# Kernel optimization log

Hardware: AMD Instinct MI355X
Metric: run time of the kernel (lower is better)

The kernel has to match this reference:

```python
import jax, jax.numpy as jnp
import numpy as np

B, S, D, H = 2, 2048, 1024, 16
DK = D // H


def setup_inputs() -> dict:
    key = jax.random.key(0)
    ks = jax.random.split(key, 12)
    sd = 1.0 / np.sqrt(D)
    inp = {
        "query": jax.random.normal(ks[0], (B, S, D), jnp.float32),
        "key": jax.random.normal(ks[1], (B, S, D), jnp.float32),
        "value": jax.random.normal(ks[2], (B, S, D), jnp.float32),
        # causal mask, broadcast over batch and heads: [1, 1, S, S]
        "mask": jnp.tril(jnp.ones((S, S), jnp.bool_))[None, None],
        "wq_w": jax.random.uniform(ks[3], (D, D), jnp.float32, -sd, sd),
        "wq_b": jax.random.uniform(ks[4], (D,), jnp.float32, -sd, sd),
        "wk_w": jax.random.uniform(ks[5], (D, D), jnp.float32, -sd, sd),
        "wk_b": jax.random.uniform(ks[6], (D,), jnp.float32, -sd, sd),
        "wv_w": jax.random.uniform(ks[7], (D, D), jnp.float32, -sd, sd),
        "wv_b": jax.random.uniform(ks[8], (D,), jnp.float32, -sd, sd),
        "wo_w": jax.random.uniform(ks[9], (D, D), jnp.float32, -sd, sd),
        "wo_b": jax.random.uniform(ks[10], (D,), jnp.float32, -sd, sd),
    }
    return inp


def reference(query, key, value, mask, wq_w, wq_b, wk_w, wk_b, wv_w, wv_b, wo_w, wo_b):
    # linear projections (torch Linear: x @ W^T + b), split into heads -> [B, H, S, DK]
    def proj(x, w, b):
        y = jnp.einsum("bsd,ed->bse", x, w) + b
        return y.reshape(B, S, H, DK).transpose(0, 2, 1, 3)

    q = proj(query, wq_w, wq_b)
    k = proj(key, wk_w, wk_b)
    v = proj(value, wv_w, wv_b)

    scale = 1.0 / np.sqrt(DK)
    scores = jnp.einsum("bhqd,bhkd->bhqk", q, k) * scale  # [B, H, S, S]
    scores = jnp.where(mask, scores, -jnp.inf)
    attn = jax.nn.softmax(scores, axis=-1)
    out = jnp.einsum("bhqk,bhkd->bhqd", attn, v)  # [B, H, S, DK]
    out = out.transpose(0, 2, 1, 3).reshape(B, S, D)
    # output projection; dropout is identity at eval / p=0
    return jnp.einsum("bsd,ed->bse", out, wo_w) + wo_b
```

## Files before the change

### kernel.cpp

```cpp
#include <hip/hip_runtime.h>


typedef unsigned short u16;
typedef unsigned int u32;
typedef __bf16 bf16x8 __attribute__((ext_vector_type(8)));
typedef float f32x4 __attribute__((ext_vector_type(4)));
typedef float f32x16 __attribute__((ext_vector_type(16)));
typedef float f32x4v __attribute__((ext_vector_type(4)));
typedef u16 u16x4 __attribute__((ext_vector_type(4)));
typedef u32 u32x4 __attribute__((ext_vector_type(4)));
typedef int i32x4 __attribute__((ext_vector_type(4)));

#define B_ 2
#define S_ 2048
#define D_ 1024
#define H_ 16
#define DK_ 64

__device__ __forceinline__ u16 f2bf(float f) {
  __bf16 h = (__bf16)f;
  return __builtin_bit_cast(u16, h);
}
__device__ __forceinline__ float fexp2(float x) { return __builtin_amdgcn_exp2f(x); }

__device__ __forceinline__ f32x4 mfma16(bf16x8 a, bf16x8 b, f32x4 c) {
  return __builtin_amdgcn_mfma_f32_16x16x32_bf16(a, b, c, 0, 0, 0);
}
__device__ __forceinline__ f32x16 mfma32(bf16x8 a, bf16x8 b, f32x16 c) {
  return __builtin_amdgcn_mfma_f32_32x32x16_bf16(a, b, c, 0, 0, 0);
}
__device__ __forceinline__ u32 cvtpk(float lo, float hi) {
  u32 r;
  asm volatile("v_cvt_pk_bf16_f32 %0, %1, %2" : "=v"(r) : "v"(lo), "v"(hi));
  return r;
}
__device__ __forceinline__ u32 sx32(u32 v) { return (u32)__shfl_xor((int)v, 32, 64); }

typedef __attribute__((address_space(1))) void GV;
typedef __attribute__((address_space(3))) void LV;
__device__ __forceinline__ void gload16(const u16* g, u16* l) {
  __builtin_amdgcn_global_load_lds((GV*)g, (LV*)l, 16, 0, 0);
}

__global__ __launch_bounds__(256) void cast_all(const float* __restrict__ s0, const float* __restrict__ s1,
                                                const float* __restrict__ s2, const float* __restrict__ s3,
                                                const float* __restrict__ s4, const float* __restrict__ s5,
                                                const float* __restrict__ s6, u16* __restrict__ dst) {
  const int N0 = 1048576, N1 = 2097152, N2 = 3145728, N3 = 3407872, N4 = 3670016, N5 = 3932160, N6 = 4194304;
  int stride = gridDim.x * blockDim.x;
  for (int i = blockIdx.x * blockDim.x + threadIdx.x; i < N6; i += stride) {
    const float* src;
    int off;
    if (i < N0)      { src = s0; off = i; }
    else if (i < N1) { src = s1; off = i - N0; }
    else if (i < N2) { src = s2; off = i - N1; }
    else if (i < N3) { src = s3; off = i - N2; }
    else if (i < N4) { src = s4; off = i - N3; }
    else if (i < N5) { src = s5; off = i - N4; }
    else             { src = s6; off = i - N5; }
    f32x4v v = reinterpret_cast<const f32x4v*>(src)[off];
    u16x4 o;
    o.x = f2bf(v.x); o.y = f2bf(v.y); o.z = f2bf(v.z); o.w = f2bf(v.w);
    reinterpret_cast<u16x4*>(dst)[i] = o;
  }
}

__device__ __forceinline__ void gemm_tile_128(const u16* __restrict__ A,
                                              const u16* __restrict__ Bw,
                                              int K, int bm, int bn,
                                              f32x4 (&acc)[4][4],
                                              u16* ldsA, u16* ldsB) {
  const int tid = threadIdx.x;
  const int lane = tid & 63;
  const int w = tid >> 6;
  const int wm = w >> 1, wn = w & 1;
  const int fr = lane & 15, fq = lane >> 4;

  const u16* aBase = A + (size_t)(bm * 128) * K;
  const u16* bBase = Bw + (size_t)(bn * 128) * K;

  const int r0 = tid >> 2;
  const int cq0 = tid & 3;
  const int cs0 = (cq0 ^ (r0 & 3)) * 8;
  const int cs1 = (cq0 ^ ((r0 + 64) & 3)) * 8;

#define STAGE_G(buf, kk)                                                                          \
  do {                                                                                            \
    gload16(aBase + (size_t)r0 * K + (kk) + cs0, ldsA + (buf) * 4096 + tid * 8);                  \
    gload16(aBase + (size_t)(r0 + 64) * K + (kk) + cs1, ldsA + (buf) * 4096 + (tid + 256) * 8);   \
    gload16(bBase + (size_t)r0 * K + (kk) + cs0, ldsB + (buf) * 4096 + tid * 8);                  \
    gload16(bBase + (size_t)(r0 + 64) * K + (kk) + cs1, ldsB + (buf) * 4096 + (tid + 256) * 8);   \
  } while (0)

  STAGE_G(0, 0);
  STAGE_G(1, 32);

  const int nk = K >> 5;
  for (int t = 0; t < nk; ++t) {
    if (t + 1 < nk) { asm volatile("s_waitcnt vmcnt(4)" ::: "memory"); }
    else            { asm volatile("s_waitcnt vmcnt(0)" ::: "memory"); }
    __builtin_amdgcn_s_barrier();
    __builtin_amdgcn_sched_barrier(0);
    if (t + 2 < nk) {
      const int nb = (t + 2) % 3;
      STAGE_G(nb, (t + 2) * 32);
    }
    const u16* la = ldsA + (t % 3) * 4096;
    const u16* lb = ldsB + (t % 3) * 4096;
    bf16x8 af[4], bfv[4];
#pragma unroll
    for (int m = 0; m < 4; ++m) {
      int row = wm * 64 + m * 16 + fr;
      int cq = fq ^ (row & 3);
      af[m] = *reinterpret_cast<const bf16x8*>(la + (row * 4 + cq) * 8);
    }
#pragma unroll
    for (int n = 0; n < 4; ++n) {
      int row = wn * 64 + n * 16 + fr;
      int cq = fq ^ (row & 3);
      bfv[n] = *reinterpret_cast<const bf16x8*>(lb + (row * 4 + cq) * 8);
    }
    __builtin_amdgcn_s_setprio(1);
#pragma unroll
    for (int m = 0; m < 4; ++m)
#pragma unroll
      for (int n = 0; n < 4; ++n)
        acc[m][n] = mfma16(af[m], bfv[n], acc[m][n]);
    __builtin_amdgcn_s_setprio(0);
  }
#undef STAGE_G
}

__global__ __launch_bounds__(256) void gemm_qkv(const u16* __restrict__ Xq, const u16* __restrict__ Xk,
                                                const u16* __restrict__ Xv, const u16* __restrict__ Wq,
                                                const u16* __restrict__ Wk, const u16* __restrict__ Wv,
                                                const float* __restrict__ bq, const float* __restrict__ bk,
                                                const float* __restrict__ bv,
                                                u16* __restrict__ Qw, u16* __restrict__ Kw,
                                                u16* __restrict__ Vt) {
  __shared__ __align__(16) u16 lds[6 * 128 * 32];
  u16* ldsA = lds;
  u16* ldsB = lds + 3 * 128 * 32;

  const int id = blockIdx.x;
  const int xcd = id & 7;
  const int l = id >> 3;
  const int bx = l & 7;
  const int g = xcd * 12 + (l >> 3);
  const int z = g >> 5;
  const int by = g & 31;

  const u16* A = (z == 0) ? Xq : (z == 1) ? Xk : Xv;
  const u16* W = (z == 0) ? Wq : (z == 1) ? Wk : Wv;
  const float* bias = (z == 0) ? bq : (z == 1) ? bk : bv;
  const float osc = (z == 0) ? (0.125f * 1.44269504f) : 1.0f;

  f32x4 acc[4][4];
#pragma unroll
  for (int m = 0; m < 4; ++m)
#pragma unroll
    for (int n = 0; n < 4; ++n)
      acc[m][n] = (f32x4){0.f, 0.f, 0.f, 0.f};

  gemm_tile_128(A, W, 1024, by, bx, acc, ldsA, ldsB);

  const int tid = threadIdx.x;
  const int lane = tid & 63;
  const int w = tid >> 6, wm = w >> 1, wn = w & 1;
  const int fr = lane & 15, fq = lane >> 4;

  __syncthreads();

  if (z < 2) {
#pragma unroll
    for (int m = 0; m < 4; ++m)
#pragma unroll
      for (int n = 0; n < 4; ++n) {
        int col = wn * 64 + n * 16 + fr;
        float bcol = bias[bx * 128 + col];
#pragma unroll
        for (int j = 0; j < 4; ++j) {
          int row = wm * 64 + m * 16 + fq * 4 + j;
          lds[row * 128 + col] = f2bf((acc[m][n][j] + bcol) * osc);
        }
      }
    __syncthreads();
    u16* dst = (z == 0) ? Qw : Kw;
#pragma unroll
    for (int p = 0; p < 8; ++p) {
      int lrow = p * 16 + (tid >> 4);
      int lseg = tid & 15;
      i32x4 v = *reinterpret_cast<const i32x4*>(&lds[lrow * 128 + lseg * 8]);
      int grow = by * 128 + lrow;
      int b = grow >> 11, s = grow & (S_ - 1);
      int h = bx * 2 + (lseg >> 3);
      int dk = (lseg & 7) * 8;
      *reinterpret_cast<i32x4*>(&dst[((size_t)(b * H_ + h) * S_ + s) * DK_ + dk]) = v;
    }
  } else {
#pragma unroll
    for (int m = 0; m < 4; ++m)
#pragma unroll
      for (int n = 0; n < 4; ++n) {
        int col = wn * 64 + n * 16 + fr;
        float bcol = bias[bx * 128 + col];
        int row0 = wm * 64 + m * 16 + fq * 4;
        u16x4 pk;
#pragma unroll
        for (int j = 0; j < 4; ++j) pk[j] = f2bf(acc[m][n][j] + bcol);
        *reinterpret_cast<u16x4*>(&lds[col * 136 + row0]) = pk;
      }
    __syncthreads();
#pragma unroll
    for (int p = 0; p < 8; ++p) {
      int dkl = p * 16 + (tid >> 4);
      int seg = tid & 15;
      i32x4 v = *reinterpret_cast<const i32x4*>(&lds[dkl * 136 + seg * 8]);
      int grow = by * 128 + seg * 8;
      int b = grow >> 11, s = grow & (S_ - 1);
      int h = bx * 2 + (dkl >> 6);
      int dk = dkl & 63;
      *reinterpret_cast<i32x4*>(&Vt[((size_t)(b * H_ + h) * DK_ + dk) * S_ + s]) = v;
    }
  }
}

__global__ __launch_bounds__(256) void gemm_out(const u16* __restrict__ O, const u16* __restrict__ Wo,
                                                const float* __restrict__ bo, float* __restrict__ Y) {
  __shared__ __align__(16) u16 ldsA[3 * 128 * 32];
  __shared__ __align__(16) u16 ldsB[3 * 128 * 32];
  const int id = blockIdx.x;
  const int xcd = id & 7;
  const int l = id >> 3;
  const int bx = l & 7;
  const int by = xcd * 4 + (l >> 3);

  f32x4 acc[4][4];
#pragma unroll
  for (int m = 0; m < 4; ++m)
#pragma unroll
    for (int n = 0; n < 4; ++n)
      acc[m][n] = (f32x4){0.f, 0.f, 0.f, 0.f};

  gemm_tile_128(O, Wo, 1024, by, bx, acc, ldsA, ldsB);

  const int lane = threadIdx.x & 63;
  const int w = threadIdx.x >> 6, wm = w >> 1, wn = w & 1;
  const int fr = lane & 15, fq = lane >> 4;
#pragma unroll
  for (int m = 0; m < 4; ++m) {
#pragma unroll
    for (int n = 0; n < 4; ++n) {
      int col = bx * 128 + wn * 64 + n * 16 + fr;
      float bcol = bo[col];
#pragma unroll
      for (int j = 0; j < 4; ++j) {
        int row = by * 128 + wm * 64 + m * 16 + fq * 4 + j;
        Y[(size_t)row * D_ + col] = acc[m][n][j] + bcol;
      }
    }
  }
}

__global__ __launch_bounds__(256, 3) void attn_kernel(const u16* __restrict__ Qw,
                                                      const u16* __restrict__ Kw,
                                                      const u16* __restrict__ Vt,
                                                      u16* __restrict__ Ob) {
  __shared__ __align__(16) u16 Kl[3][64 * 64];
  __shared__ __align__(16) u16 Vl[3][64 * 64];
  __shared__ float lls[4][32];

  const int id = blockIdx.x;
  const int bh = (id & 7) * 4 + ((id >> 3) & 3);
  const int chunk = 15 - (id >> 5);
  const int tid = threadIdx.x;
  const int w = tid >> 6;
  const int lane = tid & 63;
  const int col = lane & 31;
  const int hi = lane >> 5;

  const u16* Kg = Kw + (size_t)bh * S_ * DK_;
  const u16* Vg = Vt + (size_t)bh * DK_ * S_;
  const int b = bh >> 4, h = bh & 15;

  const int qbase = chunk * 128 + w * 32;
  const int tdiag = qbase >> 6;
  const int nt = 2 * chunk + 2;

  const u16* Qg = Qw + ((size_t)bh * S_ + qbase) * DK_;
  bf16x8 qf[4];
#pragma unroll
  for (int c = 0; c < 4; ++c)
    qf[c] = *reinterpret_cast<const bf16x8*>(Qg + col * DK_ + c * 16 + hi * 8);

  f32x16 o[2];
  float ll = 0.f;
#pragma unroll
  for (int dt = 0; dt < 2; ++dt)
#pragma unroll
    for (int r = 0; r < 16; ++r) o[dt][r] = 0.f;

  const int sr = tid >> 3;
  const int scol = ((tid & 7) ^ (sr & 7)) * 8;

#define STAGE_A(buf, t)                                                              \
  do {                                                                               \
    gload16(Kg + (size_t)((t) * 64 + sr) * DK_ + scol, &Kl[buf][tid * 8]);           \
    gload16(Kg + (size_t)((t) * 64 + sr + 32) * DK_ + scol, &Kl[buf][(tid + 256) * 8]); \
    gload16(Vg + (size_t)sr * S_ + (t) * 64 + scol, &Vl[buf][tid * 8]);              \
    gload16(Vg + (size_t)(sr + 32) * S_ + (t) * 64 + scol, &Vl[buf][(tid + 256) * 8]); \
  } while (0)

  STAGE_A(0, 0);
  STAGE_A(1, 1);

  for (int t = 0; t < nt; ++t) {
    if (t + 1 < nt) { asm volatile("s_waitcnt vmcnt(4)" ::: "memory"); }
    else            { asm volatile("s_waitcnt vmcnt(0)" ::: "memory"); }
    __builtin_amdgcn_s_barrier();
    __builtin_amdgcn_sched_barrier(0);
    if (t + 2 < nt) STAGE_A((t + 2) % 3, t + 2);

    if (t <= tdiag) {
      const u16* kl = Kl[t % 3];
      const u16* vl = Vl[t % 3];
      bf16x8 pa[4];
#pragma unroll
      for (int kt = 0; kt < 2; ++kt) {
        bf16x8 ka[4];
#pragma unroll
        for (int c = 0; c < 4; ++c) {
          int row = kt * 32 + col;
          int e = (row * 64 + c * 16 + hi * 8) ^ ((row & 7) << 3);
          ka[c] = *reinterpret_cast<const bf16x8*>(kl + e);
        }
        f32x16 s;
#pragma unroll
        for (int r = 0; r < 16; ++r) s[r] = 0.f;
        __builtin_amdgcn_s_setprio(1);
#pragma unroll
        for (int c = 0; c < 4; ++c) s = mfma32(ka[c], qf[c], s);
        __builtin_amdgcn_s_setprio(0);

        if (t == tdiag) {
#pragma unroll
          for (int r = 0; r < 16; ++r) {
            int krow = t * 64 + kt * 32 + (r & 3) + 8 * (r >> 2) + 4 * hi;
            if (krow > qbase + col) s[r] = -1.0e30f;
          }
        }
#pragma unroll
        for (int r = 0; r < 16; ++r) { s[r] = fexp2(s[r]); ll += s[r]; }

        {
          u32 g0 = cvtpk(s[0], s[1]),   g1 = cvtpk(s[2], s[3]);
          u32 g2 = cvtpk(s[4], s[5]),   g3 = cvtpk(s[6], s[7]);
          u32 g4 = cvtpk(s[8], s[9]),   g5 = cvtpk(s[10], s[11]);
          u32 g6 = cvtpk(s[12], s[13]), g7 = cvtpk(s[14], s[15]);
          u32 x0 = sx32(g0), x1 = sx32(g1), x2 = sx32(g2), x3 = sx32(g3);
          u32 x4 = sx32(g4), x5 = sx32(g5), x6 = sx32(g6), x7 = sx32(g7);
          u32x4 lo4, hi4;
          lo4.x = hi ? x2 : g0;  lo4.y = hi ? x3 : g1;
          lo4.z = hi ? g2 : x0;  lo4.w = hi ? g3 : x1;
          hi4.x = hi ? x6 : g4;  hi4.y = hi ? x7 : g5;
          hi4.z = hi ? g6 : x4;  hi4.w = hi ? g7 : x5;
          pa[kt * 2 + 0] = __builtin_bit_cast(bf16x8, lo4);
          pa[kt * 2 + 1] = __builtin_bit_cast(bf16x8, hi4);
        }
      }

      __builtin_amdgcn_s_setprio(1);
#pragma unroll
      for (int dt = 0; dt < 2; ++dt) {
#pragma unroll
        for (int kc = 0; kc < 4; ++kc) {
          int row = dt * 32 + col;
          int e = (row * 64 + kc * 16 + hi * 8) ^ ((row & 7) << 3);
          bf16x8 vb = *reinterpret_cast<const bf16x8*>(vl + e);
          o[dt] = mfma32(pa[kc], vb, o[dt]);
        }
      }
      __builtin_amdgcn_s_setprio(0);
    }
  }
#undef STAGE_A

  ll += __shfl_xor(ll, 32, 64);
  if (hi == 0) lls[w][col] = ll;
  float linv[16];
#pragma unroll
  for (int r = 0; r < 16; ++r)
    linv[r] = 1.f / lls[w][(r & 3) + 8 * (r >> 2) + 4 * hi];

#pragma unroll
  for (int dt = 0; dt < 2; ++dt)
#pragma unroll
    for (int r = 0; r < 16; ++r) {
      int q = qbase + (r & 3) + 8 * (r >> 2) + 4 * hi;
      Ob[((size_t)b * S_ + q) * D_ + h * 64 + dt * 32 + col] = f2bf(o[dt][r] * linv[r]);
    }
}

extern "C" void kernel_launch(void* const* d_in, const int* in_sizes, int n_in,
                              void* d_out, int out_size, void* d_ws, size_t ws_size,
                              hipStream_t stream) {
  const float* q_in = (const float*)d_in[0];
  const float* k_in = (const float*)d_in[1];
  const float* v_in = (const float*)d_in[2];
  const float* wq = (const float*)d_in[4];
  const float* bq = (const float*)d_in[5];
  const float* wk = (const float*)d_in[6];
  const float* bk = (const float*)d_in[7];
  const float* wv = (const float*)d_in[8];
  const float* bv = (const float*)d_in[9];
  const float* wo = (const float*)d_in[10];
  const float* bo = (const float*)d_in[11];

  char* ws = (char*)d_ws;
  const size_t MB = 1024 * 1024;
  u16* Xq = (u16*)(ws + 0 * MB);
  u16* Xk = (u16*)(ws + 8 * MB);
  u16* Xv = (u16*)(ws + 16 * MB);
  u16* Wq = (u16*)(ws + 24 * MB);
  u16* Wk = (u16*)(ws + 26 * MB);
  u16* Wv = (u16*)(ws + 28 * MB);
  u16* Wo = (u16*)(ws + 30 * MB);
  u16* Qw = (u16*)(ws + 32 * MB);
  u16* Kw = (u16*)(ws + 40 * MB);
  u16* Vt = (u16*)(ws + 48 * MB);
  u16* Ob = (u16*)(ws + 0 * MB);

  cast_all<<<2048, 256, 0, stream>>>(q_in, k_in, v_in, wq, wk, wv, wo, (u16*)ws);
  gemm_qkv<<<768, 256, 0, stream>>>(Xq, Xk, Xv, Wq, Wk, Wv, bq, bk, bv, Qw, Kw, Vt);
  attn_kernel<<<512, 256, 0, stream>>>(Qw, Kw, Vt, Ob);
  gemm_out<<<256, 256, 0, stream>>>(Ob, Wo, bo, (float*)d_out);
}
```

Before: 121.0 us.

## Shrink attention blocks to 64-query tiles and split cast kernel per tensor

The attention kernel now uses 128-thread blocks that each own a 64-query tile, launching twice as many blocks. Every staged key/value tile is then useful to both waves, so the per-wave diagonal skip goes away and the causal workload is spread more finely. The staging loop and the vmcnt wait are adjusted for the smaller block. The cast kernel gets a 2D grid with one tensor per grid row, which removes the per-element source selection branches. The trade-off is more blocks, each loading K/V with fewer threads, and possibly more total K/V traffic.

Measured after the change: 120.1 us. No clear change (-0.8%).

```diff
diff --git a/kernel.cpp b/kernel.cpp
--- a/kernel.cpp
+++ b/kernel.cpp
@@ -46,22 +46,24 @@
                                                 const float* __restrict__ s2, const float* __restrict__ s3,
                                                 const float* __restrict__ s4, const float* __restrict__ s5,
                                                 const float* __restrict__ s6, u16* __restrict__ dst) {
-  const int N0 = 1048576, N1 = 2097152, N2 = 3145728, N3 = 3407872, N4 = 3670016, N5 = 3932160, N6 = 4194304;
+  const int y = blockIdx.y;
+  const float* src;
+  int n4, base;
+  switch (y) {
+    case 0: src = s0; n4 = 1048576; base = 0; break;
+    case 1: src = s1; n4 = 1048576; base = 1048576; break;
+    case 2: src = s2; n4 = 1048576; base = 2097152; break;
+    case 3: src = s3; n4 = 262144; base = 3145728; break;
+    case 4: src = s4; n4 = 262144; base = 3407872; break;
+    case 5: src = s5; n4 = 262144; base = 3670016; break;
+    default: src = s6; n4 = 262144; base = 3932160; break;
+  }
   int stride = gridDim.x * blockDim.x;
-  for (int i = blockIdx.x * blockDim.x + threadIdx.x; i < N6; i += stride) {
-    const float* src;
-    int off;
-    if (i < N0)      { src = s0; off = i; }
-    else if (i < N1) { src = s1; off = i - N0; }
-    else if (i < N2) { src = s2; off = i - N1; }
-    else if (i < N3) { src = s3; off = i - N2; }
-    else if (i < N4) { src = s4; off = i - N3; }
-    else if (i < N5) { src = s5; off = i - N4; }
-    else             { src = s6; off = i - N5; }
-    f32x4v v = reinterpret_cast<const f32x4v*>(src)[off];
+  for (int i = blockIdx.x * blockDim.x + threadIdx.x; i < n4; i += stride) {
+    f32x4v v = reinterpret_cast<const f32x4v*>(src)[i];
     u16x4 o;
     o.x = f2bf(v.x); o.y = f2bf(v.y); o.z = f2bf(v.z); o.w = f2bf(v.w);
-    reinterpret_cast<u16x4*>(dst)[i] = o;
+    reinterpret_cast<u16x4*>(dst)[base + i] = o;
   }
 }
 
@@ -262,17 +264,17 @@
   }
 }
 
-__global__ __launch_bounds__(256, 3) void attn_kernel(const u16* __restrict__ Qw,
+__global__ __launch_bounds__(128, 2) void attn_kernel(const u16* __restrict__ Qw,
                                                       const u16* __restrict__ Kw,
                                                       const u16* __restrict__ Vt,
                                                       u16* __restrict__ Ob) {
   __shared__ __align__(16) u16 Kl[3][64 * 64];
   __shared__ __align__(16) u16 Vl[3][64 * 64];
-  __shared__ float lls[4][32];
+  __shared__ float lls[2][32];
 
   const int id = blockIdx.x;
   const int bh = (id & 7) * 4 + ((id >> 3) & 3);
-  const int chunk = 15 - (id >> 5);
+  const int qt = 31 - (id >> 5);
   const int tid = threadIdx.x;
   const int w = tid >> 6;
   const int lane = tid & 63;
@@ -283,9 +285,8 @@
   const u16* Vg = Vt + (size_t)bh * DK_ * S_;
   const int b = bh >> 4, h = bh & 15;
 
-  const int qbase = chunk * 128 + w * 32;
-  const int tdiag = qbase >> 6;
-  const int nt = 2 * chunk + 2;
+  const int qbase = qt * 64 + w * 32;
+  const int nt = qt + 1;
 
   const u16* Qg = Qw + ((size_t)bh * S_ + qbase) * DK_;
   bf16x8 qf[4];
@@ -300,88 +301,86 @@
 #pragma unroll
     for (int r = 0; r < 16; ++r) o[dt][r] = 0.f;
 
-  const int sr = tid >> 3;
-  const int scol = ((tid & 7) ^ (sr & 7)) * 8;
-
-#define STAGE_A(buf, t)                                                              \
-  do {                                                                               \
-    gload16(Kg + (size_t)((t) * 64 + sr) * DK_ + scol, &Kl[buf][tid * 8]);           \
-    gload16(Kg + (size_t)((t) * 64 + sr + 32) * DK_ + scol, &Kl[buf][(tid + 256) * 8]); \
-    gload16(Vg + (size_t)sr * S_ + (t) * 64 + scol, &Vl[buf][tid * 8]);              \
-    gload16(Vg + (size_t)(sr + 32) * S_ + (t) * 64 + scol, &Vl[buf][(tid + 256) * 8]); \
+#define STAGE_A(buf, t)                                                          \
+  do {                                                                           \
+    _Pragma("unroll") for (int i = 0; i < 4; ++i) {                              \
+      int idx = i * 128 + tid;                                                   \
+      int row = idx >> 3;                                                        \
+      int sc = ((idx & 7) ^ (row & 7)) * 8;                                      \
+      gload16(Kg + (size_t)((t) * 64 + row) * DK_ + sc, &Kl[buf][idx * 8]);      \
+      gload16(Vg + (size_t)row * S_ + (t) * 64 + sc, &Vl[buf][idx * 8]);         \
+    }                                                                            \
   } while (0)
 
   STAGE_A(0, 0);
   STAGE_A(1, 1);
 
   for (int t = 0; t < nt; ++t) {
-    if (t + 1 < nt) { asm volatile("s_waitcnt vmcnt(4)" ::: "memory"); }
+    if (t + 1 < nt) { asm volatile("s_waitcnt vmcnt(8)" ::: "memory"); }
     else            { asm volatile("s_waitcnt vmcnt(0)" ::: "memory"); }
     __builtin_amdgcn_s_barrier();
     __builtin_amdgcn_sched_barrier(0);
     if (t + 2 < nt) STAGE_A((t + 2) % 3, t + 2);
 
-    if (t <= tdiag) {
-      const u16* kl = Kl[t % 3];
-      const u16* vl = Vl[t % 3];
-      bf16x8 pa[4];
-#pragma unroll
-      for (int kt = 0; kt < 2; ++kt) {
-        bf16x8 ka[4];
-#pragma unroll
-        for (int c = 0; c < 4; ++c) {
-          int row = kt * 32 + col;
-          int e = (row * 64 + c * 16 + hi * 8) ^ ((row & 7) << 3);
-          ka[c] = *reinterpret_cast<const bf16x8*>(kl + e);
+    const u16* kl = Kl[t % 3];
+    const u16* vl = Vl[t % 3];
+    bf16x8 pa[4];
+#pragma unroll
+    for (int kt = 0; kt < 2; ++kt) {
+      bf16x8 ka[4];
+#pragma unroll
+      for (int c = 0; c < 4; ++c) {
+        int row = kt * 32 + col;
+        int e = (row * 64 + c * 16 + hi * 8) ^ ((row & 7) << 3);
+        ka[c] = *reinterpret_cast<const bf16x8*>(kl + e);
+      }
+      f32x16 s;
+#pragma unroll
+      for (int r = 0; r < 16; ++r) s[r] = 0.f;
+      __builtin_amdgcn_s_setprio(1);
+#pragma unroll
+      for (int c = 0; c < 4; ++c) s = mfma32(ka[c], qf[c], s);
+      __builtin_amdgcn_s_setprio(0);
+
+      if (t == qt) {
+#pragma unroll
+        for (int r = 0; r < 16; ++r) {
+          int krow = t * 64 + kt * 32 + (r & 3) + 8 * (r >> 2) + 4 * hi;
+          if (krow > qbase + col) s[r] = -1.0e30f;
         }
-        f32x16 s;
-#pragma unroll
-        for (int r = 0; r < 16; ++r) s[r] = 0.f;
-        __builtin_amdgcn_s_setprio(1);
-#pragma unroll
-        for (int c = 0; c < 4; ++c) s = mfma32(ka[c], qf[c], s);
-        __builtin_amdgcn_s_setprio(0);
-
-        if (t == tdiag) {
-#pragma unroll
-          for (int r = 0; r < 16; ++r) {
-            int krow = t * 64 + kt * 32 + (r & 3) + 8 * (r >> 2) + 4 * hi;
-            if (krow > qbase + col) s[r] = -1.0e30f;
-          }
-        }
-#pragma unroll
-        for (int r = 0; r < 16; ++r) { s[r] = fexp2(s[r]); ll += s[r]; }
-
-        {
-          u32 g0 = cvtpk(s[0], s[1]),   g1 = cvtpk(s[2], s[3]);
-          u32 g2 = cvtpk(s[4], s[5]),   g3 = cvtpk(s[6], s[7]);
-          u32 g4 = cvtpk(s[8], s[9]),   g5 = cvtpk(s[10], s[11]);
-          u32 g6 = cvtpk(s[12], s[13]), g7 = cvtpk(s[14], s[15]);
-          u32 x0 = sx32(g0), x1 = sx32(g1), x2 = sx32(g2), x3 = sx32(g3);
-          u32 x4 = sx32(g4), x5 = sx32(g5), x6 = sx32(g6), x7 = sx32(g7);
-          u32x4 lo4, hi4;
-          lo4.x = hi ? x2 : g0;  lo4.y = hi ? x3 : g1;
-          lo4.z = hi ? g2 : x0;  lo4.w = hi ? g3 : x1;
-          hi4.x = hi ? x6 : g4;  hi4.y = hi ? x7 : g5;
-          hi4.z = hi ? g6 : x4;  hi4.w = hi ? g7 : x5;
-          pa[kt * 2 + 0] = __builtin_bit_cast(bf16x8, lo4);
-          pa[kt * 2 + 1] = __builtin_bit_cast(bf16x8, hi4);
-        }
-      }
-
-      __builtin_amdgcn_s_setprio(1);
-#pragma unroll
-      for (int dt = 0; dt < 2; ++dt) {
-#pragma unroll
-        for (int kc = 0; kc < 4; ++kc) {
-          int row = dt * 32 + col;
-          int e = (row * 64 + kc * 16 + hi * 8) ^ ((row & 7) << 3);
-          bf16x8 vb = *reinterpret_cast<const bf16x8*>(vl + e);
-          o[dt] = mfma32(pa[kc], vb, o[dt]);
-        }
-      }
-      __builtin_amdgcn_s_setprio(0);
-    }
+      }
+#pragma unroll
+      for (int r = 0; r < 16; ++r) { s[r] = fexp2(s[r]); ll += s[r]; }
+
+      {
+        u32 g0 = cvtpk(s[0], s[1]),   g1 = cvtpk(s[2], s[3]);
+        u32 g2 = cvtpk(s[4], s[5]),   g3 = cvtpk(s[6], s[7]);
+        u32 g4 = cvtpk(s[8], s[9]),   g5 = cvtpk(s[10], s[11]);
+        u32 g6 = cvtpk(s[12], s[13]), g7 = cvtpk(s[14], s[15]);
+        u32 x0 = sx32(g0), x1 = sx32(g1), x2 = sx32(g2), x3 = sx32(g3);
+        u32 x4 = sx32(g4), x5 = sx32(g5), x6 = sx32(g6), x7 = sx32(g7);
+        u32x4 lo4, hi4;
+        lo4.x = hi ? x2 : g0;  lo4.y = hi ? x3 : g1;
+        lo4.z = hi ? g2 : x0;  lo4.w = hi ? g3 : x1;
+        hi4.x = hi ? x6 : g4;  hi4.y = hi ? x7 : g5;
+        hi4.z = hi ? g6 : x4;  hi4.w = hi ? g7 : x5;
+        pa[kt * 2 + 0] = __builtin_bit_cast(bf16x8, lo4);
+        pa[kt * 2 + 1] = __builtin_bit_cast(bf16x8, hi4);
+      }
+    }
+
+    __builtin_amdgcn_s_setprio(1);
+#pragma unroll
+    for (int dt = 0; dt < 2; ++dt) {
+#pragma unroll
+      for (int kc = 0; kc < 4; ++kc) {
+        int row = dt * 32 + col;
+        int e = (row * 64 + kc * 16 + hi * 8) ^ ((row & 7) << 3);
+        bf16x8 vb = *reinterpret_cast<const bf16x8*>(vl + e);
+        o[dt] = mfma32(pa[kc], vb, o[dt]);
+      }
+    }
+    __builtin_amdgcn_s_setprio(0);
   }
 #undef STAGE_A
 
@@ -430,8 +429,8 @@
   u16* Vt = (u16*)(ws + 48 * MB);
   u16* Ob = (u16*)(ws + 0 * MB);
 
-  cast_all<<<2048, 256, 0, stream>>>(q_in, k_in, v_in, wq, wk, wv, wo, (u16*)ws);
+  cast_all<<<dim3(256, 7), 256, 0, stream>>>(q_in, k_in, v_in, wq, wk, wv, wo, (u16*)ws);
   gemm_qkv<<<768, 256, 0, stream>>>(Xq, Xk, Xv, Wq, Wk, Wv, bq, bk, bv, Qw, Kw, Vt);
-  attn_kernel<<<512, 256, 0, stream>>>(Qw, Kw, Vt, Ob);
+  attn_kernel<<<1024, 128, 0, stream>>>(Qw, Kw, Vt, Ob);
   gemm_out<<<256, 256, 0, stream>>>(Ob, Wo, bo, (float*)d_out);
 }
```
